# Kernel tuning notes

Hardware: AMD Instinct MI355X
Metric: run time of the kernel (lower is better)

Reference implementation:

```python
import jax, jax.numpy as jnp
import numpy as np

HIDDEN = 1024
NUM_HEADS = 16
HEAD_DIM = HIDDEN // NUM_HEADS


def setup_inputs() -> dict:
    key = jax.random.key(0)
    k1, k2, k3 = jax.random.split(key, 3)
    x = jax.random.normal(k1, (2, 2048, HIDDEN), dtype=jnp.float32)
    # Linear weights, torch layout [out_features, in_features]
    w_qkv = jax.random.normal(k2, (3 * HIDDEN, HIDDEN), dtype=jnp.float32) * 0.02
    w_out = jax.random.normal(k3, (HIDDEN, HIDDEN), dtype=jnp.float32) * 0.02
    return {"x": x, "w_qkv": w_qkv, "w_out": w_out}


def reference(x, w_qkv, w_out):
    B, S, H = x.shape
    scale = 1.0 / HEAD_DIM ** 0.5
    qkv = jnp.einsum('bsh,oh->bso', x, w_qkv)              # [B,S,3H]
    qkv = qkv.reshape(B, S, 3, NUM_HEADS, HEAD_DIM)
    qkv = jnp.transpose(qkv, (2, 0, 3, 1, 4))               # [3,B,nh,S,hd]
    q, k, v = qkv[0], qkv[1], qkv[2]
    scores = jnp.einsum('bnsd,bntd->bnst', q, k) * scale    # [B,nh,S,S]
    attn = jax.nn.softmax(scores, axis=-1)
    out = jnp.einsum('bnst,bntd->bnsd', attn, v)            # [B,nh,S,hd]
    out = jnp.transpose(out, (0, 2, 1, 3)).reshape(B, S, H)
    return jnp.einsum('bsh,oh->bso', out, w_out)
```

## Files before the change

### kernel.cpp

```cpp
#include <hip/hip_runtime.h>
#include <stdint.h>

typedef unsigned short u16;
typedef __bf16 bf16x8 __attribute__((ext_vector_type(8)));
typedef float f32x4 __attribute__((ext_vector_type(4)));
typedef float f32x16 __attribute__((ext_vector_type(16)));
typedef unsigned u32x4 __attribute__((ext_vector_type(4)));

#define DEVI __device__ __forceinline__

typedef __attribute__((address_space(1))) void gvoid;
typedef __attribute__((address_space(3))) void lvoid;

DEVI u16 f2b(float f) {
  unsigned x = __builtin_bit_cast(unsigned, f);
  return (u16)((x + 0x7fffu + ((x >> 16) & 1u)) >> 16);
}

DEVI float exp2g(float x) { return __builtin_amdgcn_exp2f(x); }

DEVI void gload_lds16(const void* g, void* l) {
  __builtin_amdgcn_global_load_lds((gvoid*)g, (lvoid*)l, 16, 0, 0);
}

#define QSCALE 0.18033688011112042f

__global__ void cast_x(const float* __restrict__ in, u16* __restrict__ out, int n4) {
  int i = blockIdx.x * 256 + threadIdx.x;
  int stride = gridDim.x * 256;
  for (; i < n4; i += stride) {
    float4 v = ((const float4*)in)[i];
    ushort4 o;
    o.x = f2b(v.x); o.y = f2b(v.y); o.z = f2b(v.z); o.w = f2b(v.w);
    ((ushort4*)out)[i] = o;
  }
}

__global__ void cast_w(const float* __restrict__ wqkv, const float* __restrict__ wout,
                       u16* __restrict__ outb) {
  int i = blockIdx.x * 256 + threadIdx.x;
  int stride = gridDim.x * 256;
  for (; i < 1048576; i += stride) {
    const float* src = (i < 786432) ? wqkv + 4 * (long)i : wout + 4 * (long)(i - 786432);
    float4 v = *(const float4*)src;
    if (i < 262144) { v.x *= QSCALE; v.y *= QSCALE; v.z *= QSCALE; v.w *= QSCALE; }
    ushort4 o;
    o.x = f2b(v.x); o.y = f2b(v.y); o.z = f2b(v.z); o.w = f2b(v.w);
    ((ushort4*)outb)[i] = o;
  }
}

template<bool BF16OUT>
__global__ __launch_bounds__(256)
void gemm_bt(const u16* __restrict__ A, const u16* __restrict__ B, void* __restrict__ Cv,
             int M, int N, int K) {
  __shared__ u16 lA[128 * 64];
  __shared__ u16 lB[128 * 64];
  const int tid = threadIdx.x;
  const int lane = tid & 63;
  const int lr = lane & 15;
  const int lg = lane >> 4;
  const int wid = tid >> 6;
  const long bm = (long)blockIdx.y * 128;
  const long bn = (long)blockIdx.x * 128;
  const int wr = (wid >> 1) * 64;
  const int wc = (wid & 1) * 64;

  f32x4 acc[4][4];
#pragma unroll
  for (int i = 0; i < 4; ++i)
#pragma unroll
    for (int j = 0; j < 4; ++j)
      acc[i][j] = (f32x4){0.f, 0.f, 0.f, 0.f};

  for (int k0 = 0; k0 < K; k0 += 64) {
#pragma unroll
    for (int q = 0; q < 4; ++q) {
      int bi = tid + q * 256;
      int row = bi >> 3;
      int col = ((bi & 7) ^ (row & 7)) * 8;
      gload_lds16(A + (bm + row) * (long)K + k0 + col, (char*)lA + bi * 16);
    }
#pragma unroll
    for (int q = 0; q < 4; ++q) {
      int bi = tid + q * 256;
      int row = bi >> 3;
      int col = ((bi & 7) ^ (row & 7)) * 8;
      gload_lds16(B + (bn + row) * (long)K + k0 + col, (char*)lB + bi * 16);
    }
    __syncthreads();
#pragma unroll
    for (int kk = 0; kk < 2; ++kk) {
      bf16x8 af[4], bfr[4];
      int kb = kk * 4 + lg;
#pragma unroll
      for (int mi = 0; mi < 4; ++mi) {
        int row = wr + mi * 16 + lr;
        af[mi] = *(const bf16x8*)((const char*)lA + row * 128 + ((kb ^ (row & 7)) << 4));
      }
#pragma unroll
      for (int ni = 0; ni < 4; ++ni) {
        int row = wc + ni * 16 + lr;
        bfr[ni] = *(const bf16x8*)((const char*)lB + row * 128 + ((kb ^ (row & 7)) << 4));
      }
#pragma unroll
      for (int mi = 0; mi < 4; ++mi)
#pragma unroll
        for (int ni = 0; ni < 4; ++ni)
          acc[mi][ni] = __builtin_amdgcn_mfma_f32_16x16x32_bf16(af[mi], bfr[ni], acc[mi][ni], 0, 0, 0);
    }
    __syncthreads();
  }
#pragma unroll
  for (int mi = 0; mi < 4; ++mi)
#pragma unroll
    for (int ni = 0; ni < 4; ++ni)
#pragma unroll
      for (int r = 0; r < 4; ++r) {
        long row = bm + wr + mi * 16 + lg * 4 + r;
        long col = bn + wc + ni * 16 + lr;
        float v = acc[mi][ni][r];
        if (BF16OUT) ((u16*)Cv)[row * (long)N + col] = f2b(v);
        else         ((float*)Cv)[row * (long)N + col] = v;
      }
}

__global__ __launch_bounds__(512, 4)
void attn_fwd(const u16* __restrict__ qkv, u16* __restrict__ outb) {
  __shared__ char SM[33280];

  const int tid = threadIdx.x;
  const int lane = tid & 63;
  const int wid = tid >> 6;
  const int ql = lane & 31;
  const int h  = lane >> 5;
  const int th = wid >> 2;
  const int qb = wid & 3;
  const int qt = blockIdx.x;
  const int hd = blockIdx.y;
  const int b  = blockIdx.z;

  const long rowbase = (long)b * 2048;
  const int qcol = hd * 64;
  const int kcol = 1024 + hd * 64;
  const int vcol = 2048 + hd * 64;

  const int q0w = qt * 128 + qb * 32;
  bf16x8 qf[4];
  {
    const u16* qp = qkv + (rowbase + q0w + ql) * 3072 + qcol + h * 8;
#pragma unroll
    for (int dblk = 0; dblk < 4; ++dblk)
      qf[dblk] = *(const bf16x8*)(qp + dblk * 16);
  }

  float l_r = 0.f;
  f32x16 o[2];
#pragma unroll
  for (int d = 0; d < 2; ++d)
#pragma unroll
    for (int r = 0; r < 16; ++r) o[d][r] = 0.f;

  uint4 va0, va1;
  const int vv = tid - 256;
  const int vtl = (vv & 31) * 2;
  const int vd0 = ((vv >> 5) & 7) * 8;

  auto KSTAGE = [&](int buf, int t0s) {
#pragma unroll
    for (int q = 0; q < 2; ++q) {
      int bi = tid + q * 256;
      int t = bi >> 3;
      int c = ((bi & 7) ^ (t & 7)) * 8;
      gload_lds16(qkv + (rowbase + t0s + t) * 3072 + kcol + c, SM + buf * 8192 + bi * 16);
    }
  };
  auto VLOAD = [&](int t0s) {
    const u16* vp = qkv + (rowbase + t0s + vtl) * 3072 + vcol + vd0;
    va0 = *(const uint4*)vp;
    va1 = *(const uint4*)(vp + 3072);
  };
  auto VWRITE = [&](int buf) {
#pragma unroll
    for (int jj = 0; jj < 8; ++jj) {
      int d = vd0 + jj;
      unsigned lo = (((const unsigned*)&va0)[jj >> 1] >> ((jj & 1) * 16)) & 0xffffu;
      unsigned hi = (((const unsigned*)&va1)[jj >> 1] >> ((jj & 1) * 16)) & 0xffffu;
      *(unsigned*)(SM + 16384 + buf * 8192 + ((d * 128 + vtl * 2) ^ ((d & 7) << 4))) = lo | (hi << 16);
    }
  };

  if (tid < 256) KSTAGE(0, 0);
  else { VLOAD(0); VWRITE(0); }
  __syncthreads();

  for (int t0 = 0; t0 < 2048; t0 += 64) {
    const int cur = (t0 >> 6) & 1;
    const bool pre = (t0 + 64) < 2048;
    if (pre) {
      if (tid < 256) KSTAGE(cur ^ 1, t0 + 64);
      else VLOAD(t0 + 64);
    }

    f32x16 s;
#pragma unroll
    for (int r = 0; r < 16; ++r) s[r] = 0.f;
    const char* Kb = SM + cur * 8192 + (th * 32 + ql) * 128;
    __builtin_amdgcn_s_setprio(1);
#pragma unroll
    for (int kd = 0; kd < 4; ++kd) {
      bf16x8 kf = *(const bf16x8*)(Kb + (((kd * 2 + h) ^ (ql & 7)) << 4));
      s = __builtin_amdgcn_mfma_f32_32x32x16_bf16(kf, qf[kd], s, 0, 0, 0);
    }
    __builtin_amdgcn_s_setprio(0);

    float p[16];
#pragma unroll
    for (int r = 0; r < 16; ++r) p[r] = exp2g(s[r]);
    l_r += (((p[0] + p[1]) + (p[2] + p[3])) + ((p[4] + p[5]) + (p[6] + p[7])))
         + (((p[8] + p[9]) + (p[10] + p[11])) + ((p[12] + p[13]) + (p[14] + p[15])));

    unsigned w[8];
#pragma unroll
    for (int m = 0; m < 8; ++m)
      asm("v_cvt_pk_bf16_f32 %0, %1, %2" : "=v"(w[m]) : "v"(p[2 * m]), "v"(p[2 * m + 1]));

    bf16x8 pb[2];
#pragma unroll
    for (int ks = 0; ks < 2; ++ks) {
      unsigned a0 = w[4 * ks],     a2 = w[4 * ks + 2];
      unsigned a1 = w[4 * ks + 1], a3 = w[4 * ks + 3];
      asm("s_nop 1\n\tv_permlane32_swap_b32 %0, %1" : "+v"(a0), "+v"(a2));
      asm("s_nop 1\n\tv_permlane32_swap_b32 %0, %1" : "+v"(a1), "+v"(a3));
      u32x4 t; t[0] = a0; t[1] = a1; t[2] = a2; t[3] = a3;
      pb[ks] = __builtin_bit_cast(bf16x8, t);
    }

    if (pre && tid >= 256) VWRITE(cur ^ 1);

    __builtin_amdgcn_s_setprio(1);
#pragma unroll
    for (int dblk = 0; dblk < 2; ++dblk) {
      int d = dblk * 32 + ql;
      const char* Vb = SM + 16384 + cur * 8192 + d * 128;
#pragma unroll
      for (int ks = 0; ks < 2; ++ks) {
        bf16x8 vf = *(const bf16x8*)(Vb + (((th * 4 + ks * 2 + h) ^ (ql & 7)) << 4));
        o[dblk] = __builtin_amdgcn_mfma_f32_32x32x16_bf16(vf, pb[ks], o[dblk], 0, 0, 0);
      }
    }
    __builtin_amdgcn_s_setprio(0);
    __syncthreads();
  }

  float px = l_r, py = l_r;
  asm("s_nop 1\n\tv_permlane32_swap_b32 %0, %1" : "+v"(px), "+v"(py));
  float lw = l_r + (h ? px : py);

  if (th == 1) {
    char* reg = SM + qb * 8320;
#pragma unroll
    for (int dblk = 0; dblk < 2; ++dblk)
#pragma unroll
      for (int r = 0; r < 16; ++r) {
        int dl = dblk * 32 + (r & 3) + 8 * (r >> 2) + 4 * h;
        *(float*)(reg + dl * 128 + ql * 4) = o[dblk][r];
      }
    if (h == 0) *(float*)(reg + 8192 + ql * 4) = lw;
  }
  __syncthreads();
  if (th == 0) {
    const char* reg = SM + qb * 8320;
#pragma unroll
    for (int dblk = 0; dblk < 2; ++dblk)
#pragma unroll
      for (int r = 0; r < 16; ++r) {
        int dl = dblk * 32 + (r & 3) + 8 * (r >> 2) + 4 * h;
        o[dblk][r] += *(const float*)(reg + dl * 128 + ql * 4);
      }
    float inv = 1.0f / (lw + *(const float*)(reg + 8192 + ql * 4));
    long row = rowbase + q0w + ql;
#pragma unroll
    for (int dblk = 0; dblk < 2; ++dblk)
#pragma unroll
      for (int m = 0; m < 4; ++m) {
        ushort4 st;
        st.x = f2b(o[dblk][4 * m + 0] * inv);
        st.y = f2b(o[dblk][4 * m + 1] * inv);
        st.z = f2b(o[dblk][4 * m + 2] * inv);
        st.w = f2b(o[dblk][4 * m + 3] * inv);
        *(ushort4*)(outb + row * 1024 + qcol + dblk * 32 + 8 * m + 4 * h) = st;
      }
  }
}

extern "C" void kernel_launch(void* const* d_in, const int* in_sizes, int n_in,
                              void* d_out, int out_size, void* d_ws, size_t ws_size,
                              hipStream_t stream) {
  const float* x     = (const float*)d_in[0];
  const float* w_qkv = (const float*)d_in[1];
  const float* w_out = (const float*)d_in[2];
  float* out = (float*)d_out;

  char* ws = (char*)d_ws;
  u16* xb    = (u16*)(ws);
  u16* wqkvb = (u16*)(ws + 8388608);
  u16* woutb = (u16*)(ws + 14680064);
  u16* qkv   = (u16*)(ws + 16777216);
  u16* attn  = (u16*)(ws + 41943040);

  cast_x<<<1024, 256, 0, stream>>>(x, xb, 4096 * 1024 / 4);
  cast_w<<<1024, 256, 0, stream>>>(w_qkv, w_out, wqkvb);

  gemm_bt<true ><<<dim3(24, 32), 256, 0, stream>>>(xb, wqkvb, qkv, 4096, 3072, 1024);
  attn_fwd<<<dim3(16, 16, 2), 512, 0, stream>>>(qkv, attn);
  gemm_bt<false><<<dim3(8, 32), 256, 0, stream>>>(attn, woutb, out, 4096, 1024, 1024);
}
```

Measured before the change: 116.5 us.

## Deepen attention K/V prefetch pipeline with partial waitcnt barriers

Raises the K tile prefetch distance to two iterations using four LDS buffers, and double-buffers V in registers. The per-iteration __syncthreads is replaced by a targeted s_waitcnt (vmcnt(2) for K loaders, lgkmcnt(0) for V writers) plus a raw s_barrier, so in-flight global loads are not drained at every step. The loop is unrolled by four with compile-time buffer indices. LDS use grows to 48KB, which may lower the number of resident blocks per CU. The final iterations also prefetch rows past the end of the sequence, which can read outside the tensor for the last batch.

```diff
diff --git a/kernel.cpp b/kernel.cpp
--- a/kernel.cpp
+++ b/kernel.cpp
@@ -11,6 +11,8 @@
 
 typedef __attribute__((address_space(1))) void gvoid;
 typedef __attribute__((address_space(3))) void lvoid;
+
+template<int N> struct IC { static constexpr int v = N; };
 
 DEVI u16 f2b(float f) {
   unsigned x = __builtin_bit_cast(unsigned, f);
@@ -127,7 +129,7 @@
 
 __global__ __launch_bounds__(512, 4)
 void attn_fwd(const u16* __restrict__ qkv, u16* __restrict__ outb) {
-  __shared__ char SM[33280];
+  __shared__ char SM[49152];
 
   const int tid = threadIdx.x;
   const int lane = tid & 63;
@@ -144,6 +146,7 @@
   const int qcol = hd * 64;
   const int kcol = 1024 + hd * 64;
   const int vcol = 2048 + hd * 64;
+  const int TS = 64 * 3072;
 
   const int q0w = qt * 128 + qb * 32;
   bf16x8 qf[4];
@@ -161,51 +164,68 @@
 #pragma unroll
     for (int r = 0; r < 16; ++r) o[d][r] = 0.f;
 
-  uint4 va0, va1;
+  const int t_a = tid >> 3,           c_a = ((tid & 7) ^ (t_a & 7)) * 8;
+  const int bi1 = tid + 256;
+  const int t_b = bi1 >> 3,           c_b = ((bi1 & 7) ^ (t_b & 7)) * 8;
+  const int d0b = tid * 16, d1b = bi1 * 16;
+  const u16* kp0;
+  const u16* kp1;
   const int vv = tid - 256;
   const int vtl = (vv & 31) * 2;
   const int vd0 = ((vv >> 5) & 7) * 8;
-
-  auto KSTAGE = [&](int buf, int t0s) {
-#pragma unroll
-    for (int q = 0; q < 2; ++q) {
-      int bi = tid + q * 256;
-      int t = bi >> 3;
-      int c = ((bi & 7) ^ (t & 7)) * 8;
-      gload_lds16(qkv + (rowbase + t0s + t) * 3072 + kcol + c, SM + buf * 8192 + bi * 16);
+  const u16* vp;
+  uint4 vA0, vA1, vB0, vB1;
+
+  auto VWRITE = [&](char* dst, uint4 a, uint4 b) {
+    const unsigned* aw = (const unsigned*)&a;
+    const unsigned* bw = (const unsigned*)&b;
+#pragma unroll
+    for (int jj = 0; jj < 8; ++jj) {
+      unsigned val = __builtin_amdgcn_perm(bw[jj >> 1], aw[jj >> 1],
+                                           (jj & 1) ? 0x07060302u : 0x05040100u);
+      int d = vd0 + jj;
+      *(unsigned*)(dst + ((d * 128 + vtl * 2) ^ ((d & 7) << 4))) = val;
     }
   };
-  auto VLOAD = [&](int t0s) {
-    const u16* vp = qkv + (rowbase + t0s + vtl) * 3072 + vcol + vd0;
-    va0 = *(const uint4*)vp;
-    va1 = *(const uint4*)(vp + 3072);
-  };
-  auto VWRITE = [&](int buf) {
-#pragma unroll
-    for (int jj = 0; jj < 8; ++jj) {
-      int d = vd0 + jj;
-      unsigned lo = (((const unsigned*)&va0)[jj >> 1] >> ((jj & 1) * 16)) & 0xffffu;
-      unsigned hi = (((const unsigned*)&va1)[jj >> 1] >> ((jj & 1) * 16)) & 0xffffu;
-      *(unsigned*)(SM + 16384 + buf * 8192 + ((d * 128 + vtl * 2) ^ ((d & 7) << 4))) = lo | (hi << 16);
-    }
-  };
-
-  if (tid < 256) KSTAGE(0, 0);
-  else { VLOAD(0); VWRITE(0); }
-  __syncthreads();
-
-  for (int t0 = 0; t0 < 2048; t0 += 64) {
-    const int cur = (t0 >> 6) & 1;
-    const bool pre = (t0 + 64) < 2048;
-    if (pre) {
-      if (tid < 256) KSTAGE(cur ^ 1, t0 + 64);
-      else VLOAD(t0 + 64);
+
+  if (tid < 256) {
+    kp0 = qkv + (rowbase + t_a) * 3072 + kcol + c_a;
+    kp1 = qkv + (rowbase + t_b) * 3072 + kcol + c_b;
+    gload_lds16(kp0, SM + d0b);          gload_lds16(kp1, SM + d1b);
+    gload_lds16(kp0 + TS, SM + 8192 + d0b); gload_lds16(kp1 + TS, SM + 8192 + d1b);
+    kp0 += 2 * TS; kp1 += 2 * TS;
+  } else {
+    vp = qkv + (rowbase + vtl) * 3072 + vcol + vd0;
+    vA0 = *(const uint4*)vp; vA1 = *(const uint4*)(vp + 3072); vp += TS;
+    vB0 = *(const uint4*)vp; vB1 = *(const uint4*)(vp + 3072); vp += TS;
+    VWRITE(SM + 32768, vA0, vA1);
+  }
+  if (tid < 256) asm volatile("s_waitcnt vmcnt(2)" ::: "memory");
+  else           asm volatile("s_waitcnt lgkmcnt(0)" ::: "memory");
+  __builtin_amdgcn_s_barrier();
+  __builtin_amdgcn_sched_barrier(0);
+
+  auto body = [&](auto icv) {
+    constexpr int I = decltype(icv)::v;
+    char* KsCur = SM + I * 8192;
+    char* KsNxt = SM + ((I + 2) & 3) * 8192;
+    char* VsCur = SM + 32768 + (I & 1) * 8192;
+    char* VsWr  = SM + 32768 + ((I + 1) & 1) * 8192;
+
+    if (tid < 256) {
+      gload_lds16(kp0, KsNxt + d0b);
+      gload_lds16(kp1, KsNxt + d1b);
+      kp0 += TS; kp1 += TS;
+    } else {
+      if constexpr (I & 1) { vB0 = *(const uint4*)vp; vB1 = *(const uint4*)(vp + 3072); }
+      else                 { vA0 = *(const uint4*)vp; vA1 = *(const uint4*)(vp + 3072); }
+      vp += TS;
     }
 
     f32x16 s;
 #pragma unroll
     for (int r = 0; r < 16; ++r) s[r] = 0.f;
-    const char* Kb = SM + cur * 8192 + (th * 32 + ql) * 128;
+    const char* Kb = KsCur + (th * 32 + ql) * 128;
     __builtin_amdgcn_s_setprio(1);
 #pragma unroll
     for (int kd = 0; kd < 4; ++kd) {
@@ -214,16 +234,20 @@
     }
     __builtin_amdgcn_s_setprio(0);
 
-    float p[16];
-#pragma unroll
-    for (int r = 0; r < 16; ++r) p[r] = exp2g(s[r]);
-    l_r += (((p[0] + p[1]) + (p[2] + p[3])) + ((p[4] + p[5]) + (p[6] + p[7])))
-         + (((p[8] + p[9]) + (p[10] + p[11])) + ((p[12] + p[13]) + (p[14] + p[15])));
+    if (tid >= 256) {
+      if constexpr (I & 1) VWRITE(VsWr, vA0, vA1);
+      else                 VWRITE(VsWr, vB0, vB1);
+    }
+
+#pragma unroll
+    for (int r = 0; r < 16; ++r) s[r] = exp2g(s[r]);
+    l_r += (((s[0] + s[1]) + (s[2] + s[3])) + ((s[4] + s[5]) + (s[6] + s[7])))
+         + (((s[8] + s[9]) + (s[10] + s[11])) + ((s[12] + s[13]) + (s[14] + s[15])));
 
     unsigned w[8];
 #pragma unroll
     for (int m = 0; m < 8; ++m)
-      asm("v_cvt_pk_bf16_f32 %0, %1, %2" : "=v"(w[m]) : "v"(p[2 * m]), "v"(p[2 * m + 1]));
+      asm("v_cvt_pk_bf16_f32 %0, %1, %2" : "=v"(w[m]) : "v"(s[2 * m]), "v"(s[2 * m + 1]));
 
     bf16x8 pb[2];
 #pragma unroll
@@ -236,13 +260,10 @@
       pb[ks] = __builtin_bit_cast(bf16x8, t);
     }
 
-    if (pre && tid >= 256) VWRITE(cur ^ 1);
-
     __builtin_amdgcn_s_setprio(1);
 #pragma unroll
     for (int dblk = 0; dblk < 2; ++dblk) {
-      int d = dblk * 32 + ql;
-      const char* Vb = SM + 16384 + cur * 8192 + d * 128;
+      const char* Vb = VsCur + (dblk * 32 + ql) * 128;
 #pragma unroll
       for (int ks = 0; ks < 2; ++ks) {
         bf16x8 vf = *(const bf16x8*)(Vb + (((th * 4 + ks * 2 + h) ^ (ql & 7)) << 4));
@@ -250,8 +271,19 @@
       }
     }
     __builtin_amdgcn_s_setprio(0);
-    __syncthreads();
-  }
+
+    if (tid < 256) asm volatile("s_waitcnt vmcnt(2)" ::: "memory");
+    else           asm volatile("s_waitcnt lgkmcnt(0)" ::: "memory");
+    __builtin_amdgcn_s_barrier();
+    __builtin_amdgcn_sched_barrier(0);
+  };
+
+  for (int base = 0; base < 32; base += 4) {
+    body(IC<0>{}); body(IC<1>{}); body(IC<2>{}); body(IC<3>{});
+  }
+
+  if (tid < 256) asm volatile("s_waitcnt vmcnt(0)" ::: "memory");
+  __syncthreads();
 
   float px = l_r, py = l_r;
   asm("s_nop 1\n\tv_permlane32_swap_b32 %0, %1" : "+v"(px), "+v"(py));
```

Result: slower. 260.7 us (+123.7%).
